# Kernel tuning notes

Hardware: AMD Instinct MI355X
Metric: run time of the kernel (lower is better)

Reference implementation:

```python
import jax, jax.numpy as jnp
import numpy as np

LOW_THRESH = 0.3
HIGH_THRESH = 0.7
BATCH_SIZE = 256
NUM_POS = BATCH_SIZE // 2   # 128; guaranteed <= total_pos since B2=512 GT boxes are scattered positive
NUM_NEG = BATCH_SIZE - NUM_POS


def _xcycwh_to_x1y1x2y2(b):
    xc, yc, w, h = b[..., 0], b[..., 1], b[..., 2], b[..., 3]
    return jnp.stack([xc - w / 2, yc - h / 2, xc + w / 2, yc + h / 2], axis=-1)


def box_iou(box1, box2):
    # box1: (1, B1, 4), box2: (1, B2, 4) in (xc, yc, w, h) -> iou (1, B1, B2)
    area1 = box1[..., 2] * box1[..., 3]              # (1, B1)
    area2 = box2[..., 2] * box2[..., 3]              # (1, B2)
    c1 = _xcycwh_to_x1y1x2y2(box1)[:, :, None, :]    # (1, B1, 1, 4)
    c2 = _xcycwh_to_x1y1x2y2(box2)[:, None, :, :]    # (1, 1, B2, 4)
    x0 = jnp.maximum(c1[..., 0], c2[..., 0])
    y0 = jnp.maximum(c1[..., 1], c2[..., 1])
    x1 = jnp.minimum(c1[..., 2], c2[..., 2])
    y1 = jnp.minimum(c1[..., 3], c2[..., 3])
    inter = jnp.maximum(x1 - x0, 0.0) * jnp.maximum(y1 - y0, 0.0)  # (1, B1, B2)
    return inter / (area1[:, :, None] + area2[:, None, :] - inter)


def setup_inputs() -> dict:
    key = jax.random.key(0)
    k1, k2, k3, k4 = jax.random.split(key, 4)
    return {
        "input_boxes": jax.random.uniform(k1, (1, 50000, 4), dtype=jnp.float32),
        "target_boxes": jax.random.uniform(k2, (1, 512, 4), dtype=jnp.float32),
        "pos_noise": jax.random.uniform(k3, (50000,), dtype=jnp.float32),
        "neg_noise": jax.random.uniform(k4, (50000,), dtype=jnp.float32),
    }


def reference(input_boxes, target_boxes, pos_noise, neg_noise):
    ious = box_iou(input_boxes, target_boxes)        # (1, B1, B2)
    input_max_iou = jnp.max(ious, axis=2)            # (1, B1) best GT per proposal
    input_idx = jnp.argmax(ious, axis=2)             # (1, B1)
    target_idx = jnp.argmax(ious, axis=1)            # (1, B2) best proposal per GT

    pos_mask = input_max_iou[0] > HIGH_THRESH        # (B1,)
    neg_mask = input_max_iou[0] < LOW_THRESH
    # each GT's best-matching proposal is forced positive (scatter_)
    pos_mask = pos_mask.at[target_idx[0]].set(True)
    neg_mask = neg_mask.at[target_idx[0]].set(False)
    # fallback: if no negatives at all, negatives = complement of positives
    neg_mask = jnp.where(jnp.sum(neg_mask) == 0, ~pos_mask, neg_mask)

    # uniform sampling without replacement == top-k over iid uniform noise restricted to the mask
    pos_scores = jnp.where(pos_mask, pos_noise, -1.0)
    _, pos_input_idx = jax.lax.top_k(pos_scores, NUM_POS)      # (NUM_POS,)
    neg_scores = jnp.where(neg_mask, neg_noise, -1.0)
    _, neg_input_idx = jax.lax.top_k(neg_scores, NUM_NEG)      # (NUM_NEG,)

    pos_target_idx = input_idx[0][pos_input_idx]               # (NUM_POS,)
    return pos_input_idx, pos_target_idx, neg_input_idx
```

## Files before the change

kernel.cpp:

```cpp
#include <hip/hip_runtime.h>
#include <stdint.h>

#pragma clang fp contract(off)

typedef unsigned long long ull;

#define HIGHT 0.7f
#define LOWT  0.3f
#define KSEL  128
#define CAP   2048
#define MAXGT 512
#define TPB   256
#define CHUNK 64
#define TJ    64
#define SMP   66
#define NLAD  7

__device__ __constant__ float LADV[NLAD] = {0.998f, 0.99f, 0.95f, 0.8f, 0.5f, 0.25f, 0.0625f};

__device__ __forceinline__ float iou_pair(float ax0, float ay0, float ax1, float ay1, float aarea,
                                          float bx0, float by0, float bx1, float by1, float barea){
#pragma clang fp contract(off)
  float x0 = fmaxf(ax0, bx0);
  float y0 = fmaxf(ay0, by0);
  float x1 = fminf(ax1, bx1);
  float y1 = fminf(ay1, by1);
  float dx = fmaxf(x1 - x0, 0.0f);
  float dy = fmaxf(y1 - y0, 0.0f);
  float inter = dx * dy;
  float uni = (aarea + barea) - inter;
  return inter / uni;
}

__global__ __launch_bounds__(TPB)
void fused_iou(const float4* __restrict__ boxes, const float4* __restrict__ gts,
               int n1, int n2, int nblk,
               float* __restrict__ max_iou, int* __restrict__ input_idx,
               ull* __restrict__ colpart, int* __restrict__ forced,
               int* __restrict__ cnts_part,
               const float* __restrict__ pn, const float* __restrict__ nn)
{
#pragma clang fp contract(off)
  const int b = blockIdx.x, t = threadIdx.x;

  for (int x = b * TPB + t; x < n1; x += nblk * TPB) forced[x] = 0;

  __shared__ float4 gc[MAXGT];
  __shared__ float  ga[MAXGT];
  __shared__ float  smat[CHUNK * SMP];
  __shared__ float  sm[CHUNK];

  for (int j = t; j < n2; j += TPB){
    float4 g = gts[j];
    float hw = g.z * 0.5f, hh = g.w * 0.5f;
    gc[j] = make_float4(g.x - hw, g.y - hh, g.x + hw, g.y + hh);
    ga[j] = g.z * g.w;
  }
  __syncthreads();

  const int lo = b * CHUNK;
  int cr = n1 - lo; if (cr > CHUNK) cr = CHUNK; if (cr < 0) cr = 0;

  const int pi = t >> 2, q = t & 3;
  const bool valid = (pi < cr);
  float px0 = 0, py0 = 0, px1 = 0, py1 = 0, pa = 0;
  if (valid){
    float4 pb = boxes[lo + pi];
    float hw = pb.z * 0.5f, hh = pb.w * 0.5f;
    px0 = pb.x - hw; py0 = pb.y - hh; px1 = pb.x + hw; py1 = pb.y + hh;
    pa = pb.z * pb.w;
  }
  float vA = -1.0f, vB = -1.0f; int jA = 0, jB = 0;

  for (int tb = 0; tb < n2; tb += TJ){
    const int tn = min(TJ, n2 - tb);
    if (valid){
      const int jlim = tb + tn;
      int s = 0;
      for (;; s += 2){
        int j0 = tb + q + 4 * s;
        int j1 = j0 + 4;
        if (j1 < jlim){
          float4 g0 = gc[j0]; float a0 = ga[j0];
          float4 g1 = gc[j1]; float a1 = ga[j1];
          float u = iou_pair(px0, py0, px1, py1, pa, g0.x, g0.y, g0.z, g0.w, a0);
          float w = iou_pair(px0, py0, px1, py1, pa, g1.x, g1.y, g1.z, g1.w, a1);
          smat[pi * SMP + (j0 - tb)] = u;
          smat[pi * SMP + (j1 - tb)] = w;
          if (u > vA){ vA = u; jA = j0; }
          if (w > vB){ vB = w; jB = j1; }
        } else {
          if (j0 < jlim){
            float4 g0 = gc[j0]; float a0 = ga[j0];
            float u = iou_pair(px0, py0, px1, py1, pa, g0.x, g0.y, g0.z, g0.w, a0);
            smat[pi * SMP + (j0 - tb)] = u;
            if (u > vA){ vA = u; jA = j0; }
          }
          break;
        }
      }
    }
    __syncthreads();
    {
      const int jloc = t >> 2, qp = t & 3;
      if (jloc < tn){
        float cv = -1.0f; int cp = 0;
        const int p0 = qp * 16;
        const int p1 = min(p0 + 16, cr);
        for (int p = p0; p < p1; ++p){
          float v = smat[p * SMP + jloc];
          if (v > cv){ cv = v; cp = p; }
        }
        #pragma unroll
        for (int m = 1; m <= 2; m <<= 1){
          float ov = __shfl_xor(cv, m, 64);
          int   op = __shfl_xor(cp, m, 64);
          if (ov > cv || (ov == cv && op < cp)){ cv = ov; cp = op; }
        }
        if (qp == 0){
          colpart[(size_t)b * n2 + (tb + jloc)] =
            ((ull)__float_as_uint(cv) << 32) | (ull)(unsigned)~(unsigned)(lo + cp);
        }
      }
    }
    __syncthreads();
  }

  if (vB > vA || (vB == vA && jB < jA)){ vA = vB; jA = jB; }
  #pragma unroll
  for (int m = 1; m <= 2; m <<= 1){
    float ov = __shfl_xor(vA, m, 64);
    int   oj = __shfl_xor(jA, m, 64);
    if (ov > vA || (ov == vA && oj < jA)){ vA = ov; jA = oj; }
  }
  if (valid && q == 0){
    max_iou[lo + pi] = vA;
    input_idx[lo + pi] = jA;
    sm[pi] = vA;
  }
  __syncthreads();

  if (t < 64){
    const bool vld = (t < cr);
    float m = vld ? sm[t] : -1.0f;
    bool pos = vld && (m > HIGHT);
    bool nm  = vld && (m < LOWT);
    bool np  = vld && !(m > HIGHT);
    float sp = pos ? pn[lo + t] : -1.0f;
    float sn = (nm || np) ? nn[lo + t] : -1.0f;
    int c[24];
    c[0] = __popcll(__ballot(pos));
    c[1] = __popcll(__ballot(nm));
    c[2] = __popcll(__ballot(np));
    #pragma unroll
    for (int k = 0; k < NLAD; ++k){
      float L = LADV[k];
      c[3 + k]  = __popcll(__ballot(pos && sp > L));
      c[10 + k] = __popcll(__ballot(nm  && sn > L));
      c[17 + k] = __popcll(__ballot(np  && sn > L));
    }
    if (t == 0){
      #pragma unroll
      for (int k = 0; k < 24; ++k) cnts_part[b * 24 + k] = c[k];
    }
  }
}

__global__ __launch_bounds__(TPB)
void colreduce(const ull* __restrict__ colpart, int n2, int nblk,
               ull* __restrict__ colbest)
{
  const int jj = blockIdx.x, t = threadIdx.x;
  ull m = 0;
  for (int x = t; x < nblk; x += TPB){
    ull v = colpart[(size_t)x * n2 + jj];
    if (v > m) m = v;
  }
  __shared__ ull red[TPB];
  red[t] = m;
  __syncthreads();
  for (int s = TPB >> 1; s > 0; s >>= 1){
    if (t < s && red[t + s] > red[t]) red[t] = red[t + s];
    __syncthreads();
  }
  if (t == 0) colbest[jj] = red[0];
}

__global__ __launch_bounds__(512)
void fixup_kernel(const ull* __restrict__ colbest, int n1, int n2, int nblk,
                  const float* __restrict__ max_iou,
                  const float* __restrict__ pn, const float* __restrict__ nn,
                  int* __restrict__ forced, const int* __restrict__ cnts_part,
                  int* __restrict__ cnts)
{
  __shared__ int lc[26];
  const int t = threadIdx.x;
  if (t < 26) lc[t] = 0;
  __syncthreads();
  const int tot = nblk * 24;
  for (int x = t; x < tot; x += 512){
    int v = cnts_part[x];
    if (v) atomicAdd(&lc[x % 24], v);
  }
  if (t < n2){
    unsigned idx = ~(unsigned)(colbest[t] & 0xFFFFFFFFull);
    if (idx < (unsigned)n1){
      int old = atomicExch(&forced[idx], 1);
      if (old == 0){
        float m = max_iou[idx];
        if (!(m > HIGHT)){
          float sp = pn[idx];
          float sn = nn[idx];
          atomicAdd(&lc[0], 1);
          atomicAdd(&lc[2], -1);
          #pragma unroll
          for (int k = 0; k < NLAD; ++k){
            float L = LADV[k];
            if (sp > L) atomicAdd(&lc[3 + k], 1);
            if (sn > L) atomicAdd(&lc[17 + k], -1);
          }
          if (m < LOWT){
            atomicAdd(&lc[1], -1);
            #pragma unroll
            for (int k = 0; k < NLAD; ++k)
              if (sn > LADV[k]) atomicAdd(&lc[10 + k], -1);
          }
        }
      }
    }
  }
  __syncthreads();
  if (t < 26) cnts[t] = lc[t];
}

__device__ __forceinline__ float pick_tau(const int* lad, int tot){
  if (tot <= CAP) return -1.0f;
  for (int k = 0; k < NLAD; ++k)
    if (lad[k] >= KSEL) return LADV[k];
  return -1.0f;
}

__global__ __launch_bounds__(TPB)
void collect_kernel(const float* __restrict__ max_iou, const int* __restrict__ forced,
                    const float* __restrict__ pn, const float* __restrict__ nn,
                    int n1, int* __restrict__ cnts, ull* __restrict__ cand)
{
  __shared__ int s_c[24];
  const int t = threadIdx.x;
  if (t < 24) s_c[t] = cnts[t];
  __syncthreads();
  const bool fb = (s_c[1] == 0);
  const int totP = s_c[0];
  const int totN = fb ? s_c[2] : s_c[1];
  const float tauP = pick_tau(&s_c[3], totP);
  const float tauN = pick_tau(fb ? &s_c[17] : &s_c[10], totN);

  const int i = blockIdx.x * TPB + t;
  if (i >= n1) return;
  float m = max_iou[i];
  bool f = forced[i] != 0;
  bool pos = (m > HIGHT) || f;
  if (pos){
    float sc = pn[i];
    if (sc > tauP){
      int p = atomicAdd(&cnts[24], 1);
      if (p < CAP) cand[p] = ((ull)(__float_as_uint(sc) + 1u) << 32) | (ull)(unsigned)~(unsigned)i;
    }
  } else if (totP < KSEL && i < 2 * KSEL){
    int p = atomicAdd(&cnts[24], 1);
    if (p < CAP) cand[p] = (ull)(unsigned)~(unsigned)i;
  }
  bool seln = fb ? (!pos) : ((m < LOWT) && !f);
  if (seln){
    float sc = nn[i];
    if (sc > tauN){
      int p = atomicAdd(&cnts[25], 1);
      if (p < CAP) cand[CAP + p] = ((ull)(__float_as_uint(sc) + 1u) << 32) | (ull)(unsigned)~(unsigned)i;
    }
  } else if (totN < KSEL && i < 2 * KSEL){
    int p = atomicAdd(&cnts[25], 1);
    if (p < CAP) cand[CAP + p] = (ull)(unsigned)~(unsigned)i;
  }
}

__global__ __launch_bounds__(1024)
void select_kernel(const ull* __restrict__ cand, const int* __restrict__ cnts,
                   const int* __restrict__ input_idx, int* __restrict__ out)
{
  const int t = threadIdx.x;
  const bool isPos = (blockIdx.x == 0);
  __shared__ ull keys[CAP];
  int n = cnts[isPos ? 24 : 25]; if (n > CAP) n = CAP;
  for (int x = t; x < n; x += 1024)
    keys[x] = cand[(isPos ? 0 : CAP) + x];
  __syncthreads();
  ull mk[2]; int mr[2]; int ne = 0;
  for (int x = t; x < n; x += 1024){ mk[ne] = keys[x]; mr[ne] = 0; ++ne; }
  for (int o = 0; o < n; ++o){
    ull ko = keys[o];
    if (ne > 0) mr[0] += (ko > mk[0]);
    if (ne > 1) mr[1] += (ko > mk[1]);
  }
  for (int e = 0; e < ne; ++e){
    int r = mr[e];
    if (r < KSEL){
      unsigned idx = ~(unsigned)(mk[e] & 0xFFFFFFFFull);
      if (isPos){ out[r] = (int)idx; out[KSEL + r] = input_idx[idx]; }
      else        out[2 * KSEL + r] = (int)idx;
    }
  }
}

extern "C" void kernel_launch(void* const* d_in, const int* in_sizes, int n_in,
                              void* d_out, int out_size, void* d_ws, size_t ws_size,
                              hipStream_t stream){
  const float4* boxes = (const float4*)d_in[0];
  const float4* gts   = (const float4*)d_in[1];
  const float* pos_noise = (const float*)d_in[2];
  const float* neg_noise = (const float*)d_in[3];
  const int n1 = in_sizes[0] / 4;
  const int n2 = in_sizes[1] / 4;
  int* out = (int*)d_out;

  char* ws = (char*)d_ws;
  size_t off = 0;
  auto carve = [&](size_t bytes) -> char* {
    char* p = ws + off;
    off = (off + bytes + 255) & ~(size_t)255;
    return p;
  };
  const int nblk = (n1 + CHUNK - 1) / CHUNK;
  float* max_iou   = (float*)carve((size_t)n1 * 4);
  int*   input_idx = (int*)  carve((size_t)n1 * 4);
  ull*   colpart   = (ull*)  carve((size_t)nblk * n2 * 8);
  ull*   colbest   = (ull*)  carve((size_t)n2 * 8);
  int*   forced    = (int*)  carve((size_t)n1 * 4);
  int*   cnts_part = (int*)  carve((size_t)nblk * 24 * 4);
  int*   cnts      = (int*)  carve(32 * 4);
  ull*   cand      = (ull*)  carve((size_t)2 * CAP * 8);

  const int gb = (n1 + TPB - 1) / TPB;
  fused_iou<<<nblk, TPB, 0, stream>>>(boxes, gts, n1, n2, nblk,
                                      max_iou, input_idx, colpart, forced,
                                      cnts_part, pos_noise, neg_noise);
  colreduce<<<n2, TPB, 0, stream>>>(colpart, n2, nblk, colbest);
  fixup_kernel<<<1, 512, 0, stream>>>(colbest, n1, n2, nblk, max_iou,
                                      pos_noise, neg_noise, forced, cnts_part, cnts);
  collect_kernel<<<gb, TPB, 0, stream>>>(max_iou, forced, pos_noise, neg_noise,
                                         n1, cnts, cand);
  select_kernel<<<2, 1024, 0, stream>>>(cand, cnts, input_idx, out);
}
```

Before: 151.0 us.

## Retile IoU kernel and merge column reduction with fixup into one kernel

The IoU kernel now handles 32 proposals per block with 8 threads per proposal and 128-column GT tiles. The column-max tile reduce and the lane reduce are adapted to match. The separate colreduce and single-block fixup kernels are merged into one kernel. Its first n2 blocks reduce a column and apply the forced-positive count fixups with global atomics, and 24 extra blocks sum the per-block count partials in parallel. This removes one launch and the serial single-block count accumulation, but it doubles the number of IoU blocks and the size of the colpart buffer that the column reduce must read.

```diff
diff --git a/kernel.cpp b/kernel.cpp
--- a/kernel.cpp
+++ b/kernel.cpp
@@ -11,9 +11,9 @@
 #define CAP   2048
 #define MAXGT 512
 #define TPB   256
-#define CHUNK 64
-#define TJ    64
-#define SMP   66
+#define CHUNK 32
+#define TJ    128
+#define SMP   132
 #define NLAD  7
 
 __device__ __constant__ float LADV[NLAD] = {0.998f, 0.99f, 0.95f, 0.8f, 0.5f, 0.25f, 0.0625f};
@@ -37,13 +37,14 @@
                int n1, int n2, int nblk,
                float* __restrict__ max_iou, int* __restrict__ input_idx,
                ull* __restrict__ colpart, int* __restrict__ forced,
-               int* __restrict__ cnts_part,
+               int* __restrict__ cnts_part, int* __restrict__ cnts,
                const float* __restrict__ pn, const float* __restrict__ nn)
 {
 #pragma clang fp contract(off)
   const int b = blockIdx.x, t = threadIdx.x;
 
   for (int x = b * TPB + t; x < n1; x += nblk * TPB) forced[x] = 0;
+  if (b == 0 && t < 32) cnts[t] = 0;
 
   __shared__ float4 gc[MAXGT];
   __shared__ float  ga[MAXGT];
@@ -61,7 +62,7 @@
   const int lo = b * CHUNK;
   int cr = n1 - lo; if (cr > CHUNK) cr = CHUNK; if (cr < 0) cr = 0;
 
-  const int pi = t >> 2, q = t & 3;
+  const int pi = t >> 3, q = t & 7;
   const bool valid = (pi < cr);
   float px0 = 0, py0 = 0, px1 = 0, py1 = 0, pa = 0;
   if (valid){
@@ -78,8 +79,8 @@
       const int jlim = tb + tn;
       int s = 0;
       for (;; s += 2){
-        int j0 = tb + q + 4 * s;
-        int j1 = j0 + 4;
+        int j0 = tb + q + 8 * s;
+        int j1 = j0 + 8;
         if (j1 < jlim){
           float4 g0 = gc[j0]; float a0 = ga[j0];
           float4 g1 = gc[j1]; float a1 = ga[j1];
@@ -102,22 +103,19 @@
     }
     __syncthreads();
     {
-      const int jloc = t >> 2, qp = t & 3;
+      const int jloc = t >> 1, half = t & 1;
       if (jloc < tn){
         float cv = -1.0f; int cp = 0;
-        const int p0 = qp * 16;
+        const int p0 = half * 16;
         const int p1 = min(p0 + 16, cr);
         for (int p = p0; p < p1; ++p){
           float v = smat[p * SMP + jloc];
           if (v > cv){ cv = v; cp = p; }
         }
-        #pragma unroll
-        for (int m = 1; m <= 2; m <<= 1){
-          float ov = __shfl_xor(cv, m, 64);
-          int   op = __shfl_xor(cp, m, 64);
-          if (ov > cv || (ov == cv && op < cp)){ cv = ov; cp = op; }
-        }
-        if (qp == 0){
+        float ov = __shfl_xor(cv, 1, 64);
+        int   op = __shfl_xor(cp, 1, 64);
+        if (ov > cv || (ov == cv && op < cp)){ cv = ov; cp = op; }
+        if (half == 0){
           colpart[(size_t)b * n2 + (tb + jloc)] =
             ((ull)__float_as_uint(cv) << 32) | (ull)(unsigned)~(unsigned)(lo + cp);
         }
@@ -128,7 +126,7 @@
 
   if (vB > vA || (vB == vA && jB < jA)){ vA = vB; jA = jB; }
   #pragma unroll
-  for (int m = 1; m <= 2; m <<= 1){
+  for (int m = 1; m <= 4; m <<= 1){
     float ov = __shfl_xor(vA, m, 64);
     int   oj = __shfl_xor(jA, m, 64);
     if (ov > vA || (ov == vA && oj < jA)){ vA = ov; jA = oj; }
@@ -167,70 +165,68 @@
 }
 
 __global__ __launch_bounds__(TPB)
-void colreduce(const ull* __restrict__ colpart, int n2, int nblk,
-               ull* __restrict__ colbest)
+void colfix_kernel(const ull* __restrict__ colpart, int n1, int n2, int nblk,
+                   const float* __restrict__ max_iou,
+                   const float* __restrict__ pn, const float* __restrict__ nn,
+                   int* __restrict__ forced, const int* __restrict__ cnts_part,
+                   int* __restrict__ cnts)
 {
-  const int jj = blockIdx.x, t = threadIdx.x;
-  ull m = 0;
-  for (int x = t; x < nblk; x += TPB){
-    ull v = colpart[(size_t)x * n2 + jj];
-    if (v > m) m = v;
-  }
+  const int t = threadIdx.x;
   __shared__ ull red[TPB];
-  red[t] = m;
-  __syncthreads();
-  for (int s = TPB >> 1; s > 0; s >>= 1){
-    if (t < s && red[t + s] > red[t]) red[t] = red[t + s];
+  __shared__ int ired[TPB];
+
+  if (blockIdx.x < (unsigned)n2){
+    const int jj = blockIdx.x;
+    ull m = 0;
+    for (int x = t; x < nblk; x += TPB){
+      ull v = colpart[(size_t)x * n2 + jj];
+      if (v > m) m = v;
+    }
+    red[t] = m;
     __syncthreads();
-  }
-  if (t == 0) colbest[jj] = red[0];
-}
-
-__global__ __launch_bounds__(512)
-void fixup_kernel(const ull* __restrict__ colbest, int n1, int n2, int nblk,
-                  const float* __restrict__ max_iou,
-                  const float* __restrict__ pn, const float* __restrict__ nn,
-                  int* __restrict__ forced, const int* __restrict__ cnts_part,
-                  int* __restrict__ cnts)
-{
-  __shared__ int lc[26];
-  const int t = threadIdx.x;
-  if (t < 26) lc[t] = 0;
-  __syncthreads();
-  const int tot = nblk * 24;
-  for (int x = t; x < tot; x += 512){
-    int v = cnts_part[x];
-    if (v) atomicAdd(&lc[x % 24], v);
-  }
-  if (t < n2){
-    unsigned idx = ~(unsigned)(colbest[t] & 0xFFFFFFFFull);
-    if (idx < (unsigned)n1){
-      int old = atomicExch(&forced[idx], 1);
-      if (old == 0){
-        float m = max_iou[idx];
-        if (!(m > HIGHT)){
-          float sp = pn[idx];
-          float sn = nn[idx];
-          atomicAdd(&lc[0], 1);
-          atomicAdd(&lc[2], -1);
-          #pragma unroll
-          for (int k = 0; k < NLAD; ++k){
-            float L = LADV[k];
-            if (sp > L) atomicAdd(&lc[3 + k], 1);
-            if (sn > L) atomicAdd(&lc[17 + k], -1);
-          }
-          if (m < LOWT){
-            atomicAdd(&lc[1], -1);
+    for (int s = TPB >> 1; s > 0; s >>= 1){
+      if (t < s && red[t + s] > red[t]) red[t] = red[t + s];
+      __syncthreads();
+    }
+    if (t == 0){
+      unsigned idx = ~(unsigned)(red[0] & 0xFFFFFFFFull);
+      if (idx < (unsigned)n1){
+        int old = atomicExch(&forced[idx], 1);
+        if (old == 0){
+          float m2 = max_iou[idx];
+          if (!(m2 > HIGHT)){
+            float sp = pn[idx];
+            float sn = nn[idx];
+            atomicAdd(&cnts[0], 1);
+            atomicAdd(&cnts[2], -1);
             #pragma unroll
-            for (int k = 0; k < NLAD; ++k)
-              if (sn > LADV[k]) atomicAdd(&lc[10 + k], -1);
+            for (int k = 0; k < NLAD; ++k){
+              float L = LADV[k];
+              if (sp > L) atomicAdd(&cnts[3 + k], 1);
+              if (sn > L) atomicAdd(&cnts[17 + k], -1);
+            }
+            if (m2 < LOWT){
+              atomicAdd(&cnts[1], -1);
+              #pragma unroll
+              for (int k = 0; k < NLAD; ++k)
+                if (sn > LADV[k]) atomicAdd(&cnts[10 + k], -1);
+            }
           }
         }
       }
     }
-  }
-  __syncthreads();
-  if (t < 26) cnts[t] = lc[t];
+  } else {
+    const int k = blockIdx.x - n2;
+    int s = 0;
+    for (int x = t; x < nblk; x += TPB) s += cnts_part[x * 24 + k];
+    ired[t] = s;
+    __syncthreads();
+    for (int st = TPB >> 1; st > 0; st >>= 1){
+      if (t < st) ired[t] += ired[t + st];
+      __syncthreads();
+    }
+    if (t == 0 && ired[0]) atomicAdd(&cnts[k], ired[0]);
+  }
 }
 
 __device__ __forceinline__ float pick_tau(const int* lad, int tot){
@@ -333,7 +329,6 @@
   float* max_iou   = (float*)carve((size_t)n1 * 4);
   int*   input_idx = (int*)  carve((size_t)n1 * 4);
   ull*   colpart   = (ull*)  carve((size_t)nblk * n2 * 8);
-  ull*   colbest   = (ull*)  carve((size_t)n2 * 8);
   int*   forced    = (int*)  carve((size_t)n1 * 4);
   int*   cnts_part = (int*)  carve((size_t)nblk * 24 * 4);
   int*   cnts      = (int*)  carve(32 * 4);
@@ -342,10 +337,9 @@
   const int gb = (n1 + TPB - 1) / TPB;
   fused_iou<<<nblk, TPB, 0, stream>>>(boxes, gts, n1, n2, nblk,
                                       max_iou, input_idx, colpart, forced,
-                                      cnts_part, pos_noise, neg_noise);
-  colreduce<<<n2, TPB, 0, stream>>>(colpart, n2, nblk, colbest);
-  fixup_kernel<<<1, 512, 0, stream>>>(colbest, n1, n2, nblk, max_iou,
-                                      pos_noise, neg_noise, forced, cnts_part, cnts);
+                                      cnts_part, cnts, pos_noise, neg_noise);
+  colfix_kernel<<<n2 + 24, TPB, 0, stream>>>(colpart, n1, n2, nblk, max_iou,
+                                             pos_noise, neg_noise, forced, cnts_part, cnts);
   collect_kernel<<<gb, TPB, 0, stream>>>(max_iou, forced, pos_noise, neg_noise,
                                          n1, cnts, cand);
   select_kernel<<<2, 1024, 0, stream>>>(cand, cnts, input_idx, out);
```

Result: faster. 136.1 us, median of 2 (-9.9%).
